# Optimization experiments

Hardware: AMD Instinct MI355X
Metric: run time of the kernel (lower is better)

## Reference

```python
import jax, jax.numpy as jnp
import numpy as np

NUM_HEADS = 8
RMS_EPS = 1e-8


def rmsnorm(x, g):
    return x * jax.lax.rsqrt(jnp.mean(x * x, axis=-1, keepdims=True) + RMS_EPS) * g


def activation_quant(x):
    # per-token int8 absmax quant
    scale = 127.0 / jnp.clip(jnp.max(jnp.abs(x), axis=-1, keepdims=True), 1e-5)
    return jnp.clip(jnp.round(x * scale), -128, 127) / scale


def weight_quant(w):
    # ternary (1.58-bit) mean-absmax quant
    scale = 1.0 / jnp.clip(jnp.mean(jnp.abs(w)), 1e-5)
    return jnp.clip(jnp.round(w * scale), -1, 1) / scale


def bitlinear(x, w, g):
    # BitLinear: RMSNorm -> STE-quantized activation @ STE-quantized ternary weight
    xn = rmsnorm(x, g)
    xq = xn + jax.lax.stop_gradient(activation_quant(xn) - xn)
    wq = w + jax.lax.stop_gradient(weight_quant(w) - w)
    return xq @ wq.T


def _attention_pass(q_in, ctx, Wq, gq, Wkv, gkv, A, Bm, mag, Wp, gp):
    B, Nq, C = q_in.shape
    H = NUM_HEADS
    hd = C // H
    scale = hd ** -0.5
    q_proj = bitlinear(q_in, Wq, gq)                       # [B,Nq,C]
    delta = (q_in @ A.T) @ Bm.T                            # DoRA low-rank delta [B,Nq,C]
    q = q_proj.reshape(B, Nq, H, hd).transpose(0, 2, 1, 3)  # [B,H,Nq,hd]
    d = delta.reshape(B, Nq, H, hd).transpose(0, 2, 1, 3)
    q_final = q + mag * d                                  # mag: [1,H,1,1]
    kv = bitlinear(ctx, Wkv, gkv)                          # [B,Nc,2C]
    k, v = jnp.split(kv, 2, axis=-1)
    Nc = ctx.shape[1]
    k = k.reshape(B, Nc, H, hd).transpose(0, 2, 1, 3)
    v = v.reshape(B, Nc, H, hd).transpose(0, 2, 1, 3)
    scores = jnp.einsum('bhqd,bhkd->bhqk', q_final, k) * scale
    out = jnp.einsum('bhqk,bhkd->bhqd', jax.nn.softmax(scores, axis=-1), v)
    out = out.transpose(0, 2, 1, 3).reshape(B, Nq, C)
    return bitlinear(out, Wp, gp)


def setup_inputs() -> dict:
    key = jax.random.key(0)
    ks = jax.random.split(key, 20)
    B, Nx, Nc, D, R = 4, 4096, 1024, 512, 16
    H = NUM_HEADS

    def rn(k, shape, s=0.02):
        return jax.random.normal(k, shape, dtype=jnp.float32) * s

    return {
        'x': jax.random.normal(ks[0], (B, Nx, D), dtype=jnp.float32),
        'c': jax.random.normal(ks[1], (B, Nc, D), dtype=jnp.float32),
        # x-queries-on-c pass
        'W_qx': rn(ks[2], (D, D)), 'g_qx': jnp.ones((D,), jnp.float32),
        'W_kvc': rn(ks[3], (2 * D, D)), 'g_kvc': jnp.ones((D,), jnp.float32),
        'A_x': rn(ks[4], (R, D)), 'B_x': rn(ks[5], (D, R)),
        'mag_x': jnp.ones((1, H, 1, 1), jnp.float32),
        'W_px': rn(ks[6], (D, D)), 'g_px': jnp.ones((D,), jnp.float32),
        # c-queries-on-x pass
        'W_qc': rn(ks[7], (D, D)), 'g_qc': jnp.ones((D,), jnp.float32),
        'W_kvx': rn(ks[8], (2 * D, D)), 'g_kvx': jnp.ones((D,), jnp.float32),
        'A_c': rn(ks[9], (R, D)), 'B_c': rn(ks[10], (D, R)),
        'mag_c': jnp.ones((1, H, 1, 1), jnp.float32),
        'W_pc': rn(ks[11], (D, D)), 'g_pc': jnp.ones((D,), jnp.float32),
    }


def reference(x, c, W_qx, g_qx, W_kvc, g_kvc, A_x, B_x, mag_x, W_px, g_px,
              W_qc, g_qc, W_kvx, g_kvx, A_c, B_c, mag_c, W_pc, g_pc):
    x_out = x + _attention_pass(x, c, W_qx, g_qx, W_kvc, g_kvc, A_x, B_x, mag_x, W_px, g_px)
    c_out = c + _attention_pass(c, x, W_qc, g_qc, W_kvx, g_kvx, A_c, B_c, mag_c, W_pc, g_pc)
    return (x_out, c_out)
```

## Files before the change

### kernel.cpp

```cpp
#include <hip/hip_runtime.h>
#include <math.h>

#define DD 512
#define NHEAD 8
#define HDIM 64

typedef __bf16 bf16x8 __attribute__((ext_vector_type(8)));
typedef unsigned short u16x8 __attribute__((ext_vector_type(8)));
typedef float f32x4 __attribute__((ext_vector_type(4)));
typedef int i32x4 __attribute__((ext_vector_type(4)));
typedef signed char i8x8 __attribute__((ext_vector_type(8)));

#if __has_builtin(__builtin_amdgcn_exp2f)
#define EXP2F(x) __builtin_amdgcn_exp2f(x)
#else
#define EXP2F(x) exp2f(x)
#endif

#define QSCALE 0.18033688f

static __device__ __forceinline__ unsigned short f2bf(float f) {
    unsigned u = __builtin_bit_cast(unsigned, f);
    u += 0x7fffu + ((u >> 16) & 1u);
    return (unsigned short)(u >> 16);
}
static __device__ __forceinline__ float bf2f(unsigned short u) {
    return __builtin_bit_cast(float, (unsigned)u << 16);
}

static __device__ __forceinline__ float wsum32(const float* __restrict__ part, int mid) {
    int l = threadIdx.x & 63;
    float v = (l < 32) ? part[mid * 32 + l] : 0.f;
#pragma unroll
    for (int o = 16; o > 0; o >>= 1) v += __shfl_xor(v, o);
    return __shfl(v, 0);
}

#define GLOAD16(g, l)                                                          \
    __builtin_amdgcn_global_load_lds(                                          \
        (__attribute__((address_space(1))) void*)(g),                          \
        (__attribute__((address_space(3))) void*)(l), 16, 0, 0)

#define BSTEP(s, hc)                                                           \
    {                                                                          \
        _Pragma("unroll")                                                      \
        for (int i = 0; i < (hc); ++i) {                                       \
            float send = (lane & (s)) ? p[i] : p[i + (hc)];                    \
            float recv = __shfl_xor(send, (s));                                \
            p[i] = ((lane & (s)) ? p[i + (hc)] : p[i]) + recv;                 \
        }                                                                      \
    }

#define ISSUE_TILE(Aq, Wq, m0, n0, k0, slot)                                   \
    {                                                                          \
        _Pragma("unroll")                                                      \
        for (int i = 0; i < 2; ++i)                                            \
            GLOAD16(Aq + (size_t)((m0) + i * 128 + row_st) * 512 + (k0) + chunk * 16, \
                    sA[slot] + ((size_t)i * 512 + t) * 16);                    \
        GLOAD16(Wq + (size_t)((n0) + row_st) * 512 + (k0) + chunk * 16,        \
                sB[slot] + (size_t)t * 16);                                    \
    }

#define GEMM_KLOOP_I8(Aq, Wq, m0, n0)                                          \
    {                                                                          \
        ISSUE_TILE(Aq, Wq, m0, n0, 0, 0)                                       \
        ISSUE_TILE(Aq, Wq, m0, n0, 64, 1)                                      \
        asm volatile("s_waitcnt vmcnt(3)" ::: "memory");                       \
        __builtin_amdgcn_s_barrier();                                          \
        _Pragma("unroll")                                                      \
        for (int step = 0; step < 8; ++step) {                                 \
            if (step + 2 < 8)                                                  \
                ISSUE_TILE(Aq, Wq, m0, n0, (step + 2) * 64, (step + 2) % 3)    \
            const int cs = step % 3;                                           \
            i32x4 af[4], bfr[4];                                               \
            _Pragma("unroll")                                                  \
            for (int mt = 0; mt < 4; ++mt)                                     \
                af[mt] = *reinterpret_cast<const i32x4*>(                      \
                    &sA[cs][(wm * 64 + mt * 16 + lr) * 64 + lg * 16]);         \
            _Pragma("unroll")                                                  \
            for (int nt = 0; nt < 4; ++nt)                                     \
                bfr[nt] = *reinterpret_cast<const i32x4*>(                     \
                    &sB[cs][(wn * 64 + nt * 16 + lr) * 64 + lg * 16]);         \
            __builtin_amdgcn_s_setprio(1);                                     \
            _Pragma("unroll")                                                  \
            for (int mt = 0; mt < 4; ++mt)                                     \
                _Pragma("unroll")                                              \
                for (int nt = 0; nt < 4; ++nt)                                 \
                    acc[mt][nt] = __builtin_amdgcn_mfma_i32_16x16x64_i8(       \
                        af[mt], bfr[nt], acc[mt][nt], 0, 0, 0);                \
            __builtin_amdgcn_s_setprio(0);                                     \
            if (step < 7) {                                                    \
                if (step < 6)                                                  \
                    asm volatile("s_waitcnt vmcnt(3)" ::: "memory");           \
                else                                                           \
                    asm volatile("s_waitcnt vmcnt(0)" ::: "memory");           \
                __builtin_amdgcn_s_barrier();                                  \
            }                                                                  \
        }                                                                      \
    }

__global__ __launch_bounds__(256) void k_prep1(
    const float* __restrict__ W0, const float* __restrict__ W1,
    const float* __restrict__ W2, const float* __restrict__ W3,
    const float* __restrict__ W4, const float* __restrict__ W5,
    float* __restrict__ part,
    const float* __restrict__ x, const float* __restrict__ c,
    const float* __restrict__ g_qx, const float* __restrict__ g_kvx,
    const float* __restrict__ g_qc, const float* __restrict__ g_kvc,
    signed char* __restrict__ a_xq, signed char* __restrict__ a_xkv,
    signed char* __restrict__ a_cq, signed char* __restrict__ a_ckv,
    float* __restrict__ s_xq, float* __restrict__ s_xkv,
    float* __restrict__ s_cq, float* __restrict__ s_ckv,
    const float* __restrict__ A_x, const float* __restrict__ A_c,
    float* __restrict__ tmp_x, float* __restrict__ tmp_c) {
    int t = threadIdx.x;
    if (blockIdx.x < 192) {
        const float* Ws[6] = {W0, W1, W2, W3, W4, W5};
        const int cnt[6] = {262144, 524288, 262144, 262144, 524288, 262144};
        int mid = blockIdx.x >> 5, lb = blockIdx.x & 31;
        const float* W = Ws[mid];
        int n = cnt[mid];
        float s = 0.f;
        for (int i = lb * 256 + t; i < n; i += 32 * 256) s += fabsf(W[i]);
        __shared__ float red[4];
#pragma unroll
        for (int o = 32; o > 0; o >>= 1) s += __shfl_down(s, o);
        if ((t & 63) == 0) red[t >> 6] = s;
        __syncthreads();
        if (t == 0) part[blockIdx.x] = red[0] + red[1] + red[2] + red[3];
        return;
    }
    int w = t >> 6, lane = t & 63;
    int row = (int)(blockIdx.x - 192) * 4 + w;
    bool pc = (row >= 16384);
    int r = pc ? row - 16384 : row;
    const float* xr = (pc ? c : x) + (size_t)r * DD;
    const float* G1 = pc ? g_qc : g_qx;
    const float* G2 = pc ? g_kvc : g_kvx;
    signed char* O1 = pc ? a_cq : a_xq;
    signed char* O2 = pc ? a_ckv : a_xkv;
    float* S1 = pc ? s_cq : s_xq;
    float* S2 = pc ? s_ckv : s_xkv;
    const float* AM = pc ? A_c : A_x;
    float* TMP = pc ? tmp_c : tmp_x;

    float4 a = *(const float4*)(xr + lane * 8);
    float4 b = *(const float4*)(xr + lane * 8 + 4);
    float p[16];
#pragma unroll
    for (int cc = 0; cc < 16; ++cc) {
        const float4* ar = (const float4*)(AM + (size_t)cc * DD + lane * 8);
        float4 aa = ar[0], ab = ar[1];
        p[cc] = a.x*aa.x + a.y*aa.y + a.z*aa.z + a.w*aa.w
              + b.x*ab.x + b.y*ab.y + b.z*ab.z + b.w*ab.w;
    }
    BSTEP(1, 8) BSTEP(2, 4) BSTEP(4, 2) BSTEP(8, 1)
    p[0] += __shfl_xor(p[0], 16);
    p[0] += __shfl_xor(p[0], 32);
    if (lane < 16) {
        int cidx = ((lane & 1) << 3) | ((lane & 2) << 1) | ((lane & 4) >> 1) | ((lane & 8) >> 3);
        TMP[(size_t)r * 16 + cidx] = p[0];
    }
    float ss = a.x*a.x + a.y*a.y + a.z*a.z + a.w*a.w
             + b.x*b.x + b.y*b.y + b.z*b.z + b.w*b.w;
#pragma unroll
    for (int o = 32; o > 0; o >>= 1) ss += __shfl_xor(ss, o);
    float rn = 1.f / sqrtf(ss * (1.f / 512.f) + 1e-8f);
    const float* gs[2] = {G1, G2};
    signed char* os[2] = {O1, O2};
    float* scs[2] = {S1, S2};
#pragma unroll
    for (int pass = 0; pass < 2; ++pass) {
        float4 ga = *(const float4*)(gs[pass] + lane * 8);
        float4 gb = *(const float4*)(gs[pass] + lane * 8 + 4);
        float v[8] = {a.x*rn*ga.x, a.y*rn*ga.y, a.z*rn*ga.z, a.w*rn*ga.w,
                      b.x*rn*gb.x, b.y*rn*gb.y, b.z*rn*gb.z, b.w*rn*gb.w};
        float amax = 0.f;
#pragma unroll
        for (int i = 0; i < 8; ++i) amax = fmaxf(amax, fabsf(v[i]));
#pragma unroll
        for (int o = 32; o > 0; o >>= 1) amax = fmaxf(amax, __shfl_xor(amax, o));
        float mx = fmaxf(amax, 1e-5f);
        float scale = 127.f / mx;
        i8x8 qv;
#pragma unroll
        for (int i = 0; i < 8; ++i) {
            float tq = rintf(v[i] * scale);
            tq = fminf(fmaxf(tq, -128.f), 127.f);
            qv[i] = (signed char)(int)tq;
        }
        *reinterpret_cast<i8x8*>(os[pass] + (size_t)r * DD + lane * 8) = qv;
        if (lane == 0) scs[pass][r] = mx / 127.f;
    }
}

__global__ __launch_bounds__(256) void k_prep2(
    const float* __restrict__ W0, const float* __restrict__ W1,
    const float* __restrict__ W2, const float* __restrict__ W3,
    const float* __restrict__ W4, const float* __restrict__ W5,
    const float* __restrict__ part, signed char* __restrict__ Wq,
    const float* __restrict__ tmp_x, const float* __restrict__ tmp_c,
    const float* __restrict__ B_x, const float* __restrict__ B_c,
    unsigned short* __restrict__ qf1, unsigned short* __restrict__ qf2) {
    if (blockIdx.x < 8192) {
        int e = blockIdx.x * 256 + threadIdx.x;
        const float* Ws[6] = {W0, W1, W2, W3, W4, W5};
        int mid, base;
        if (e < 262144)       { mid = 0; base = 0; }
        else if (e < 786432)  { mid = 1; base = 262144; }
        else if (e < 1048576) { mid = 2; base = 786432; }
        else if (e < 1310720) { mid = 3; base = 1048576; }
        else if (e < 1835008) { mid = 4; base = 1310720; }
        else                  { mid = 5; base = 1835008; }
        float cnt = (mid == 1 || mid == 4) ? 524288.f : 262144.f;
        float mean = fmaxf(wsum32(part, mid) / cnt, 1e-5f);
        float sc = 1.f / mean;
        float t = rintf(Ws[mid][e - base] * sc);
        t = fminf(fmaxf(t, -1.f), 1.f);
        Wq[e] = (signed char)(int)t;
        return;
    }
    int idx = (int)(blockIdx.x - 8192) * 256 + threadIdx.x;
    int m2 = idx >> 9, n2 = idx & 511;
    const float* tr;
    const float* br;
    unsigned short* out;
    if (m2 < 16384) {
        tr = tmp_x + (size_t)m2 * 16; br = B_x + (size_t)n2 * 16; out = qf1 + idx;
    } else {
        tr = tmp_c + (size_t)(m2 - 16384) * 16; br = B_c + (size_t)n2 * 16;
        out = qf2 + (idx - 8388608);
    }
    const float4* t4 = (const float4*)tr;
    const float4* b4 = (const float4*)br;
    float acc = 0.f;
#pragma unroll
    for (int rr = 0; rr < 4; ++rr) {
        float4 ta = t4[rr], ba = b4[rr];
        acc += ta.x*ba.x + ta.y*ba.y + ta.z*ba.z + ta.w*ba.w;
    }
    *out = f2bf(acc);
}

__global__ __launch_bounds__(256) void k_rmsq_combine(
    const unsigned short* __restrict__ Op_a, const float* __restrict__ Lp_a,
    const float* __restrict__ g_a, signed char* __restrict__ out_a,
    float* __restrict__ sc_a,
    const unsigned short* __restrict__ Op_b, const float* __restrict__ Lp_b,
    const float* __restrict__ g_b, signed char* __restrict__ out_b,
    float* __restrict__ sc_b) {
    int w = threadIdx.x >> 6, lane = threadIdx.x & 63;
    int row = (int)blockIdx.x * 4 + w;
    bool pb = (row >= 16384);
    int r = pb ? row - 16384 : row;
    int S = pb ? 4 : 1;
    int lognq = pb ? 10 : 12;
    const unsigned short* Op = pb ? Op_b : Op_a;
    const float* Lp = pb ? Lp_b : Lp_a;
    const float* g  = pb ? g_b : g_a;
    signed char* out = pb ? out_b : out_a;
    float* a_inv = pb ? sc_b : sc_a;

    int Nq = 1 << lognq;
    int b = r >> lognq, q = r & (Nq - 1);
    int h = lane >> 3;
    float l = 0.f;
    float u[8] = {};
    for (int s = 0; s < S; ++s) {
        l += Lp[((size_t)(s * 4 + b) * 8 + h) * Nq + q];
        u16x8 ov = *reinterpret_cast<const u16x8*>(
            Op + ((size_t)(s * 4 + b) * Nq + q) * 512 + lane * 8);
#pragma unroll
        for (int i = 0; i < 8; ++i) u[i] += bf2f(ov[i]);
    }
    float invl = 1.f / l;
#pragma unroll
    for (int i = 0; i < 8; ++i) u[i] *= invl;
    float ss = 0.f;
#pragma unroll
    for (int i = 0; i < 8; ++i) ss += u[i] * u[i];
#pragma unroll
    for (int o = 32; o > 0; o >>= 1) ss += __shfl_xor(ss, o);
    float rn = 1.f / sqrtf(ss * (1.f / 512.f) + 1e-8f);
    float4 ga = *(const float4*)(g + lane * 8);
    float4 gb = *(const float4*)(g + lane * 8 + 4);
    float v[8] = {u[0]*rn*ga.x, u[1]*rn*ga.y, u[2]*rn*ga.z, u[3]*rn*ga.w,
                  u[4]*rn*gb.x, u[5]*rn*gb.y, u[6]*rn*gb.z, u[7]*rn*gb.w};
    float amax = 0.f;
#pragma unroll
    for (int i = 0; i < 8; ++i) amax = fmaxf(amax, fabsf(v[i]));
#pragma unroll
    for (int o = 32; o > 0; o >>= 1) amax = fmaxf(amax, __shfl_xor(amax, o));
    float mx = fmaxf(amax, 1e-5f);
    float scale = 127.f / mx;
    i8x8 qv;
#pragma unroll
    for (int i = 0; i < 8; ++i) {
        float tq = rintf(v[i] * scale);
        tq = fminf(fmaxf(tq, -128.f), 127.f);
        qv[i] = (signed char)(int)tq;
    }
    *reinterpret_cast<i8x8*>(out + (size_t)r * DD + lane * 8) = qv;
    if (lane == 0) a_inv[r] = mx / 127.f;
}

__global__ __launch_bounds__(512) void k_gemm_qkv(
    const signed char* __restrict__ a3_a, const signed char* __restrict__ a3_b,
    const signed char* __restrict__ w3_a, const signed char* __restrict__ w3_b,
    const float* __restrict__ ai3_a, const float* __restrict__ ai3_b,
    const float* __restrict__ mag_a, const float* __restrict__ mag_b,
    const unsigned short* __restrict__ dl_a, const unsigned short* __restrict__ dl_b,
    unsigned short* __restrict__ Qb_a, unsigned short* __restrict__ Qb_b,
    const signed char* __restrict__ a4_a, const signed char* __restrict__ a4_b,
    const signed char* __restrict__ w4_a, const signed char* __restrict__ w4_b,
    const float* __restrict__ ai4_a, const float* __restrict__ ai4_b,
    unsigned short* __restrict__ Kb_a, unsigned short* __restrict__ Kb_b,
    unsigned short* __restrict__ Vt_a, unsigned short* __restrict__ Vt_b,
    const float* __restrict__ part) {
    __shared__ __align__(16) unsigned char sA[3][256 * 64];
    __shared__ __align__(16) unsigned char sB[3][128 * 64];
    int bid = blockIdx.x;
    bool isQ = (bid >= 640);
    const signed char *Aq, *Wq;
    const float* a_inv;
    int m0, n0, logn, mid;
    float cnt;
    bool pb;
    if (!isQ) {
        int g = bid & 7, k = bid >> 3;
        n0 = (k & 7) * 128;
        int my = (k >> 3) * 8 + g;
        pb = my >= 16;
        m0 = (pb ? my - 16 : my) * 256;
        Aq = pb ? a4_b : a4_a;  Wq = pb ? w4_b : w4_a;
        a_inv = pb ? ai4_b : ai4_a;
        logn = pb ? 12 : 10;
        mid = pb ? 4 : 1; cnt = 524288.f;
    } else {
        int b2 = bid - 640;
        int g = b2 & 7, k = b2 >> 3;
        n0 = (k & 3) * 128;
        int my = (k >> 2) * 8 + g;
        pb = my >= 64;
        m0 = (pb ? my - 64 : my) * 256;
        Aq = pb ? a3_b : a3_a;  Wq = pb ? w3_b : w3_a;
        a_inv = pb ? ai3_b : ai3_a;
        logn = pb ? 10 : 12;
        mid = pb ? 3 : 0; cnt = 262144.f;
    }
    float wv = fmaxf(wsum32(part, mid) / cnt, 1e-5f);

    int t = threadIdx.x;
    int w = t >> 6, lane = t & 63;
    int wm = w >> 1, wn = w & 1;
    int lr = lane & 15, lg = lane >> 4;
    int row_st = t >> 2, chunk = t & 3;
    i32x4 acc[4][4] = {};

    GEMM_KLOOP_I8(Aq, Wq, m0, n0)

    if (!isQ) {
        unsigned short* OutB = pb ? Kb_b : Kb_a;
        unsigned short* OutB2 = pb ? Vt_b : Vt_a;
        const bool isV = (n0 >= 512);
        const int Nc = 1 << logn;
#pragma unroll
        for (int mt = 0; mt < 4; ++mt) {
            int mb = m0 + wm * 64 + mt * 16 + lg * 4;
            int b = mb >> logn, key = mb & (Nc - 1);
            float as_[4];
#pragma unroll
            for (int r = 0; r < 4; ++r) as_[r] = a_inv[mb + r] * wv;
#pragma unroll
            for (int nt = 0; nt < 4; ++nt) {
                int n = n0 + wn * 64 + nt * 16 + lr;
                int n2 = isV ? (n - 512) : n;
                int h = n2 >> 6, dd = n2 & 63;
                if (isV) {
                    int i0 = key & 31;
                    int keyp = (key & ~31) | (((i0 >> 2) & 3) * 8 + ((i0 >> 4) & 1) * 4);
                    ushort4 v;
                    v.x = f2bf((float)acc[mt][nt][0] * as_[0]);
                    v.y = f2bf((float)acc[mt][nt][1] * as_[1]);
                    v.z = f2bf((float)acc[mt][nt][2] * as_[2]);
                    v.w = f2bf((float)acc[mt][nt][3] * as_[3]);
                    *reinterpret_cast<ushort4*>(
                        OutB2 + ((size_t)(b * NHEAD + h) * 64 + dd) * Nc + keyp) = v;
                } else {
#pragma unroll
                    for (int r = 0; r < 4; ++r)
                        OutB[((size_t)(b * NHEAD + h) * Nc + key + r) * 64 + dd] =
                            f2bf((float)acc[mt][nt][r] * as_[r]);
                }
            }
        }
    } else {
        const float* Extra = pb ? mag_b : mag_a;
        const unsigned short* Dlt = pb ? dl_b : dl_a;
        unsigned short* OutB = pb ? Qb_b : Qb_a;
#pragma unroll
        for (int mt = 0; mt < 4; ++mt) {
#pragma unroll
            for (int r = 0; r < 4; ++r) {
                int m = m0 + wm * 64 + mt * 16 + lg * 4 + r;
                float as = a_inv[m] * wv;
                int b = m >> logn, q = m & ((1 << logn) - 1);
#pragma unroll
                for (int nt = 0; nt < 4; ++nt) {
                    int n = n0 + wn * 64 + nt * 16 + lr;
                    float dl = bf2f(Dlt[(size_t)m * 512 + n]);
                    float val = (float)acc[mt][nt][r] * as + Extra[n >> 6] * dl;
                    int h = n >> 6, d = n & 63;
                    OutB[((((size_t)(b * NHEAD + h)) << logn) + q) * 64 + d] =
                        f2bf(val * QSCALE);
                }
            }
        }
    }
}

__global__ __launch_bounds__(512) void k_gemm_out(
    const signed char* __restrict__ a_a, const signed char* __restrict__ a_b,
    const signed char* __restrict__ w_a, const signed char* __restrict__ w_b,
    const float* __restrict__ ai_a, const float* __restrict__ ai_b,
    const float* __restrict__ part,
    const float* __restrict__ Ex_a, const float* __restrict__ Ex_b,
    float* __restrict__ OF_a, float* __restrict__ OF_b) {
    __shared__ __align__(16) unsigned char sA[3][256 * 64];
    __shared__ __align__(16) unsigned char sB[3][128 * 64];
    int bid = blockIdx.x;
    int g = bid & 7, k = bid >> 3;
    int n0 = (k & 3) * 128;
    int my = (k >> 2) * 8 + g;
    bool pb = (my >= 64);
    int m0 = (pb ? my - 64 : my) * 256;
    const signed char* Aq = pb ? a_b : a_a;
    const signed char* Wq = pb ? w_b : w_a;
    const float* a_inv = pb ? ai_b : ai_a;
    const float* Extra = pb ? Ex_b : Ex_a;
    float* OutF = pb ? OF_b : OF_a;
    float wv = fmaxf(wsum32(part, pb ? 5 : 2) / 262144.f, 1e-5f);

    int t = threadIdx.x;
    int w = t >> 6, lane = t & 63;
    int wm = w >> 1, wn = w & 1;
    int lr = lane & 15, lg = lane >> 4;
    int row_st = t >> 2, chunk = t & 3;
    i32x4 acc[4][4] = {};

    GEMM_KLOOP_I8(Aq, Wq, m0, n0)

#pragma unroll
    for (int mt = 0; mt < 4; ++mt) {
#pragma unroll
        for (int r = 0; r < 4; ++r) {
            int m = m0 + wm * 64 + mt * 16 + lg * 4 + r;
            float as = a_inv[m] * wv;
#pragma unroll
            for (int nt = 0; nt < 4; ++nt) {
                int n = n0 + wn * 64 + nt * 16 + lr;
                size_t idx = (size_t)m * 512 + n;
                OutF[idx] = (float)acc[mt][nt][r] * as + Extra[idx];
            }
        }
    }
}

__global__ __launch_bounds__(512) void k_attn_mfma(
    const unsigned short* __restrict__ Qb_a, const unsigned short* __restrict__ Kb_a,
    const unsigned short* __restrict__ Vt_a, unsigned short* __restrict__ Op_a,
    float* __restrict__ Lp_a,
    const unsigned short* __restrict__ Qb_b, const unsigned short* __restrict__ Kb_b,
    const unsigned short* __restrict__ Vt_b, unsigned short* __restrict__ Op_b,
    float* __restrict__ Lp_b) {
    __shared__ unsigned short sK[2][64][72];
    __shared__ unsigned short sVt[2][64][72];
    int t = threadIdx.x;
    int w = t >> 6, lane = t & 63;
    int lr = lane & 15, lg = lane >> 4;

    int bid = blockIdx.x;
    bool pb = (bid < 512);
    int lb = pb ? bid : bid - 512;
    const unsigned short* Qb = pb ? Qb_b : Qb_a;
    const unsigned short* Kb = pb ? Kb_b : Kb_a;
    const unsigned short* Vt = pb ? Vt_b : Vt_a;
    unsigned short* Opart = pb ? Op_b : Op_a;
    float* Lpart = pb ? Lp_b : Lp_a;
    int Nq = pb ? 1024 : 4096;
    int Nc = pb ? 4096 : 1024;
    int S = pb ? 4 : 1;
    int LOGS = pb ? 2 : 0;
    int nqs = pb ? 2 : 4;

    int j = lb >> 3;
    int s = j & (S - 1);
    int j2 = j >> LOGS;
    int qblk = j2 & ((1 << nqs) - 1);
    int bh = ((lb & 7) << 2) | (j2 >> nqs);
    int b = bh >> 3, h = bh & 7;
    int q0 = qblk * 256 + w * 32;

    bf16x8 aq[2][2];
#pragma unroll
    for (int qt = 0; qt < 2; ++qt) {
        const unsigned short* qbase = Qb + ((size_t)bh * Nq + q0 + qt * 16 + lr) * 64 + lg * 8;
        aq[qt][0] = *reinterpret_cast<const bf16x8*>(qbase);
        aq[qt][1] = *reinterpret_cast<const bf16x8*>(qbase + 32);
    }

    u16x8 ou;
#pragma unroll
    for (int jj = 0; jj < 8; ++jj) ou[jj] = (lr == 0) ? 0x3F80 : 0;
    bf16x8 onesf = __builtin_bit_cast(bf16x8, ou);

    f32x4 o[2][4] = {};
    f32x4 osum[2] = {};

    const unsigned short* kglob = Kb + (size_t)bh * Nc * 64;
    const unsigned short* vglob = Vt + (size_t)bh * 64 * (size_t)Nc;

    int srow = t >> 3, sseg = t & 7;
    const unsigned short* kptr = kglob + (size_t)srow * 64 + sseg * 8;
    const unsigned short* vptr = vglob + (size_t)srow * Nc + sseg * 8;

    int kts = s * (Nc >> LOGS);
    int nt = (Nc >> LOGS) >> 6;

    bf16x8 rK = *reinterpret_cast<const bf16x8*>(kptr + (size_t)kts * 64);
    bf16x8 rV = *reinterpret_cast<const bf16x8*>(vptr + kts);
    *reinterpret_cast<bf16x8*>(&sK[0][srow][sseg * 8]) = rK;
    *reinterpret_cast<bf16x8*>(&sVt[0][srow][sseg * 8]) = rV;
    rK = *reinterpret_cast<const bf16x8*>(kptr + (size_t)(kts + 64) * 64);
    rV = *reinterpret_cast<const bf16x8*>(vptr + kts + 64);
    __syncthreads();

    int cur = 0;
    for (int ti = 0; ti < nt; ++ti) {
        if (ti + 1 < nt) {
            *reinterpret_cast<bf16x8*>(&sK[cur ^ 1][srow][sseg * 8]) = rK;
            *reinterpret_cast<bf16x8*>(&sVt[cur ^ 1][srow][sseg * 8]) = rV;
            if (ti + 2 < nt) {
                int knext = kts + (ti + 2) * 64;
                rK = *reinterpret_cast<const bf16x8*>(kptr + (size_t)knext * 64);
                rV = *reinterpret_cast<const bf16x8*>(vptr + knext);
            }
        }
#pragma unroll
        for (int half = 0; half < 2; ++half) {
            bf16x8 pa0, pa1;
#pragma unroll
            for (int ki = 0; ki < 2; ++ki) {
                int kt = half * 2 + ki;
                bf16x8 bk0 = *reinterpret_cast<const bf16x8*>(&sK[cur][kt * 16 + lr][lg * 8]);
                bf16x8 bk1 = *reinterpret_cast<const bf16x8*>(&sK[cur][kt * 16 + lr][32 + lg * 8]);
                f32x4 a0 = {}, a1 = {};
                __builtin_amdgcn_s_setprio(1);
                a0 = __builtin_amdgcn_mfma_f32_16x16x32_bf16(bk0, aq[0][0], a0, 0, 0, 0);
                a1 = __builtin_amdgcn_mfma_f32_16x16x32_bf16(bk0, aq[1][0], a1, 0, 0, 0);
                a0 = __builtin_amdgcn_mfma_f32_16x16x32_bf16(bk1, aq[0][1], a0, 0, 0, 0);
                a1 = __builtin_amdgcn_mfma_f32_16x16x32_bf16(bk1, aq[1][1], a1, 0, 0, 0);
                __builtin_amdgcn_s_setprio(0);
                const int hb = ki * 4;
#pragma unroll
                for (int r = 0; r < 4; ++r) {
                    pa0[hb + r] = (__bf16)EXP2F(a0[r]);
                    pa1[hb + r] = (__bf16)EXP2F(a1[r]);
                }
            }
            __builtin_amdgcn_s_setprio(1);
#pragma unroll
            for (int dt = 0; dt < 4; ++dt) {
                bf16x8 vb = *reinterpret_cast<const bf16x8*>(&sVt[cur][dt * 16 + lr][half * 32 + lg * 8]);
                o[0][dt] = __builtin_amdgcn_mfma_f32_16x16x32_bf16(pa0, vb, o[0][dt], 0, 0, 0);
                o[1][dt] = __builtin_amdgcn_mfma_f32_16x16x32_bf16(pa1, vb, o[1][dt], 0, 0, 0);
            }
            osum[0] = __builtin_amdgcn_mfma_f32_16x16x32_bf16(pa0, onesf, osum[0], 0, 0, 0);
            osum[1] = __builtin_amdgcn_mfma_f32_16x16x32_bf16(pa1, onesf, osum[1], 0, 0, 0);
            __builtin_amdgcn_s_setprio(0);
        }
        __syncthreads();
        cur ^= 1;
    }
    unsigned short* obase = Opart + ((size_t)(s * 4 + b) * Nq + q0) * 512 + h * 64;
#pragma unroll
    for (int qt = 0; qt < 2; ++qt)
#pragma unroll
        for (int dt = 0; dt < 4; ++dt)
#pragma unroll
            for (int r = 0; r < 4; ++r)
                obase[(size_t)(qt * 16 + lg * 4 + r) * 512 + dt * 16 + lr] = f2bf(o[qt][dt][r]);
    if (lr == 0) {
        float* lbase = Lpart + ((size_t)(s * 4 + b) * 8 + h) * Nq + q0;
#pragma unroll
        for (int qt = 0; qt < 2; ++qt)
#pragma unroll
            for (int r = 0; r < 4; ++r)
                lbase[qt * 16 + lg * 4 + r] = osum[qt][r];
    }
}

extern "C" void kernel_launch(void* const* d_in, const int* in_sizes, int n_in,
                              void* d_out, int out_size, void* d_ws, size_t ws_size,
                              hipStream_t stream) {
    const float* x     = (const float*)d_in[0];
    const float* c     = (const float*)d_in[1];
    const float* Wq_x  = (const float*)d_in[2];
    const float* g_qx  = (const float*)d_in[3];
    const float* Wkv_c = (const float*)d_in[4];
    const float* g_kvc = (const float*)d_in[5];
    const float* A_x   = (const float*)d_in[6];
    const float* B_x   = (const float*)d_in[7];
    const float* mag_x = (const float*)d_in[8];
    const float* Wp_x  = (const float*)d_in[9];
    const float* g_px  = (const float*)d_in[10];
    const float* Wq_c  = (const float*)d_in[11];
    const float* g_qc  = (const float*)d_in[12];
    const float* Wkv_x = (const float*)d_in[13];
    const float* g_kvx = (const float*)d_in[14];
    const float* A_c   = (const float*)d_in[15];
    const float* B_c   = (const float*)d_in[16];
    const float* mag_c = (const float*)d_in[17];
    const float* Wp_c  = (const float*)d_in[18];
    const float* g_pc  = (const float*)d_in[19];

    float* ws = (float*)d_ws;
    signed char* Wb = (signed char*)ws;
    const size_t Woff[6] = {0, 262144, 786432, 1048576, 1310720, 1835008};
    float* part  = ws + 1048576;
    float* sc_xq  = ws + 1049600;
    float* sc_xkv = sc_xq + 16384;
    float* sc_cq  = sc_xkv + 16384;
    float* sc_ckv = sc_cq + 4096;
    float* sc_o1  = sc_ckv + 4096;
    float* sc_o2  = sc_o1 + 16384;
    float* tmp_x  = ws + 1111040;
    float* tmp_c  = tmp_x + 262144;
    float* actblk = ws + 1438720;
    signed char* act_xq  = (signed char*)actblk;
    signed char* act_xkv = (signed char*)(actblk + 4194304);
    signed char* act_cq  = (signed char*)(actblk + 8388608);
    signed char* act_ckv = (signed char*)(actblk + 9437184);
    unsigned short* Opart1 = (unsigned short*)actblk;
    float* qf1_f  = ws + 11924480;
    unsigned short* Opart2 = (unsigned short*)qf1_f;
    float* qf2_f  = ws + 16118784;
    float* Qb1_f  = ws + 17167360;
    float* Qb2_f  = ws + 21361664;
    float* Kb1_f  = ws + 22410240;
    float* Vt1_f  = ws + 23458816;
    float* Kb2_f  = ws + 24507392;
    float* Vt2_f  = ws + 28701696;
    float* Lpart1 = ws + 32896000;
    float* Lpart2 = ws + 33027072;

    unsigned short* qf1 = (unsigned short*)qf1_f;
    unsigned short* qf2 = (unsigned short*)qf2_f;
    unsigned short* Qb1 = (unsigned short*)Qb1_f;
    unsigned short* Qb2 = (unsigned short*)Qb2_f;
    unsigned short* Kb1 = (unsigned short*)Kb1_f;
    unsigned short* Vt1 = (unsigned short*)Vt1_f;
    unsigned short* Kb2 = (unsigned short*)Kb2_f;
    unsigned short* Vt2 = (unsigned short*)Vt2_f;
    signed char* act_o1 = (signed char*)Qb1;
    signed char* act_o2 = (signed char*)Qb2;

    size_t need = (size_t)33158144 * sizeof(float);
    if (ws_size < need) return;

    float* outx = (float*)d_out;
    float* outc = outx + (size_t)4 * 4096 * 512;

    k_prep1<<<5312, 256, 0, stream>>>(Wq_x, Wkv_c, Wp_x, Wq_c, Wkv_x, Wp_c, part,
                                      x, c, g_qx, g_kvx, g_qc, g_kvc,
                                      act_xq, act_xkv, act_cq, act_ckv,
                                      sc_xq, sc_xkv, sc_cq, sc_ckv,
                                      A_x, A_c, tmp_x, tmp_c);
    k_prep2<<<49152, 256, 0, stream>>>(Wq_x, Wkv_c, Wp_x, Wq_c, Wkv_x, Wp_c, part, Wb,
                                       tmp_x, tmp_c, B_x, B_c, qf1, qf2);
    k_gemm_qkv<<<960, 512, 0, stream>>>(
        act_xq, act_cq, Wb + Woff[0], Wb + Woff[3], sc_xq, sc_cq,
        mag_x, mag_c, qf1, qf2, Qb1, Qb2,
        act_ckv, act_xkv, Wb + Woff[1], Wb + Woff[4], sc_ckv, sc_xkv,
        Kb1, Kb2, Vt1, Vt2, part);
    k_attn_mfma<<<1024, 512, 0, stream>>>(Qb1, Kb1, Vt1, Opart1, Lpart1,
                                          Qb2, Kb2, Vt2, Opart2, Lpart2);
    k_rmsq_combine<<<5120, 256, 0, stream>>>(Opart1, Lpart1, g_px, act_o1, sc_o1,
                                             Opart2, Lpart2, g_pc, act_o2, sc_o2);
    k_gemm_out<<<320, 512, 0, stream>>>(
        act_o1, act_o2, Wb + Woff[2], Wb + Woff[5], sc_o1, sc_o2, part,
        x, c, outx, outc);
}
```

Before: 234.8 us.

## Double per-wave query rows in attention and compute softmax sums with VALU

Each wave now handles 64 query rows (four 16-row subtiles) instead of 32, halving the block count and reusing each K/V tile from shared memory across twice as many queries. The row-sum of exponentials is accumulated in registers with adds and cross-lane shuffles instead of extra MFMAs against a ones vector. Launch bounds request two blocks per CU. The cost is much higher register pressure (16 output accumulators plus 8 query fragments), which may cause spills or lower occupancy, and fewer blocks to balance across CUs.

```diff
diff --git a/kernel.cpp b/kernel.cpp
--- a/kernel.cpp
+++ b/kernel.cpp
@@ -466,7 +466,7 @@
     }
 }
 
-__global__ __launch_bounds__(512) void k_attn_mfma(
+__global__ __launch_bounds__(512, 2) void k_attn_mfma(
     const unsigned short* __restrict__ Qb_a, const unsigned short* __restrict__ Kb_a,
     const unsigned short* __restrict__ Vt_a, unsigned short* __restrict__ Op_a,
     float* __restrict__ Lp_a,
@@ -480,8 +480,8 @@
     int lr = lane & 15, lg = lane >> 4;
 
     int bid = blockIdx.x;
-    bool pb = (bid < 512);
-    int lb = pb ? bid : bid - 512;
+    bool pb = (bid < 256);
+    int lb = pb ? bid : bid - 256;
     const unsigned short* Qb = pb ? Qb_b : Qb_a;
     const unsigned short* Kb = pb ? Kb_b : Kb_a;
     const unsigned short* Vt = pb ? Vt_b : Vt_a;
@@ -491,7 +491,7 @@
     int Nc = pb ? 4096 : 1024;
     int S = pb ? 4 : 1;
     int LOGS = pb ? 2 : 0;
-    int nqs = pb ? 2 : 4;
+    int nqs = pb ? 1 : 3;
 
     int j = lb >> 3;
     int s = j & (S - 1);
@@ -499,23 +499,18 @@
     int qblk = j2 & ((1 << nqs) - 1);
     int bh = ((lb & 7) << 2) | (j2 >> nqs);
     int b = bh >> 3, h = bh & 7;
-    int q0 = qblk * 256 + w * 32;
-
-    bf16x8 aq[2][2];
-#pragma unroll
-    for (int qt = 0; qt < 2; ++qt) {
-        const unsigned short* qbase = Qb + ((size_t)bh * Nq + q0 + qt * 16 + lr) * 64 + lg * 8;
-        aq[qt][0] = *reinterpret_cast<const bf16x8*>(qbase);
-        aq[qt][1] = *reinterpret_cast<const bf16x8*>(qbase + 32);
-    }
-
-    u16x8 ou;
-#pragma unroll
-    for (int jj = 0; jj < 8; ++jj) ou[jj] = (lr == 0) ? 0x3F80 : 0;
-    bf16x8 onesf = __builtin_bit_cast(bf16x8, ou);
-
-    f32x4 o[2][4] = {};
-    f32x4 osum[2] = {};
+    int q0 = qblk * 512 + w * 64;
+
+    bf16x8 aq[4][2];
+#pragma unroll
+    for (int st = 0; st < 4; ++st) {
+        const unsigned short* qbase = Qb + ((size_t)bh * Nq + q0 + st * 16 + lr) * 64 + lg * 8;
+        aq[st][0] = *reinterpret_cast<const bf16x8*>(qbase);
+        aq[st][1] = *reinterpret_cast<const bf16x8*>(qbase + 32);
+    }
+
+    f32x4 o[4][4] = {};
+    float psum[4] = {0.f, 0.f, 0.f, 0.f};
 
     const unsigned short* kglob = Kb + (size_t)bh * Nc * 64;
     const unsigned short* vglob = Vt + (size_t)bh * 64 * (size_t)Nc;
@@ -548,55 +543,64 @@
         }
 #pragma unroll
         for (int half = 0; half < 2; ++half) {
-            bf16x8 pa0, pa1;
+            bf16x8 pa[4];
 #pragma unroll
             for (int ki = 0; ki < 2; ++ki) {
                 int kt = half * 2 + ki;
                 bf16x8 bk0 = *reinterpret_cast<const bf16x8*>(&sK[cur][kt * 16 + lr][lg * 8]);
                 bf16x8 bk1 = *reinterpret_cast<const bf16x8*>(&sK[cur][kt * 16 + lr][32 + lg * 8]);
-                f32x4 a0 = {}, a1 = {};
+                f32x4 a0 = {}, a1 = {}, a2 = {}, a3 = {};
                 __builtin_amdgcn_s_setprio(1);
                 a0 = __builtin_amdgcn_mfma_f32_16x16x32_bf16(bk0, aq[0][0], a0, 0, 0, 0);
                 a1 = __builtin_amdgcn_mfma_f32_16x16x32_bf16(bk0, aq[1][0], a1, 0, 0, 0);
+                a2 = __builtin_amdgcn_mfma_f32_16x16x32_bf16(bk0, aq[2][0], a2, 0, 0, 0);
+                a3 = __builtin_amdgcn_mfma_f32_16x16x32_bf16(bk0, aq[3][0], a3, 0, 0, 0);
                 a0 = __builtin_amdgcn_mfma_f32_16x16x32_bf16(bk1, aq[0][1], a0, 0, 0, 0);
                 a1 = __builtin_amdgcn_mfma_f32_16x16x32_bf16(bk1, aq[1][1], a1, 0, 0, 0);
+                a2 = __builtin_amdgcn_mfma_f32_16x16x32_bf16(bk1, aq[2][1], a2, 0, 0, 0);
+                a3 = __builtin_amdgcn_mfma_f32_16x16x32_bf16(bk1, aq[3][1], a3, 0, 0, 0);
                 __builtin_amdgcn_s_setprio(0);
                 const int hb = ki * 4;
 #pragma unroll
                 for (int r = 0; r < 4; ++r) {
-                    pa0[hb + r] = (__bf16)EXP2F(a0[r]);
-                    pa1[hb + r] = (__bf16)EXP2F(a1[r]);
+                    float e0 = EXP2F(a0[r]); psum[0] += e0; pa[0][hb + r] = (__bf16)e0;
+                    float e1 = EXP2F(a1[r]); psum[1] += e1; pa[1][hb + r] = (__bf16)e1;
+                    float e2 = EXP2F(a2[r]); psum[2] += e2; pa[2][hb + r] = (__bf16)e2;
+                    float e3 = EXP2F(a3[r]); psum[3] += e3; pa[3][hb + r] = (__bf16)e3;
                 }
             }
             __builtin_amdgcn_s_setprio(1);
 #pragma unroll
             for (int dt = 0; dt < 4; ++dt) {
                 bf16x8 vb = *reinterpret_cast<const bf16x8*>(&sVt[cur][dt * 16 + lr][half * 32 + lg * 8]);
-                o[0][dt] = __builtin_amdgcn_mfma_f32_16x16x32_bf16(pa0, vb, o[0][dt], 0, 0, 0);
-                o[1][dt] = __builtin_amdgcn_mfma_f32_16x16x32_bf16(pa1, vb, o[1][dt], 0, 0, 0);
+                o[0][dt] = __builtin_amdgcn_mfma_f32_16x16x32_bf16(pa[0], vb, o[0][dt], 0, 0, 0);
+                o[1][dt] = __builtin_amdgcn_mfma_f32_16x16x32_bf16(pa[1], vb, o[1][dt], 0, 0, 0);
+                o[2][dt] = __builtin_amdgcn_mfma_f32_16x16x32_bf16(pa[2], vb, o[2][dt], 0, 0, 0);
+                o[3][dt] = __builtin_amdgcn_mfma_f32_16x16x32_bf16(pa[3], vb, o[3][dt], 0, 0, 0);
             }
-            osum[0] = __builtin_amdgcn_mfma_f32_16x16x32_bf16(pa0, onesf, osum[0], 0, 0, 0);
-            osum[1] = __builtin_amdgcn_mfma_f32_16x16x32_bf16(pa1, onesf, osum[1], 0, 0, 0);
             __builtin_amdgcn_s_setprio(0);
         }
         __syncthreads();
         cur ^= 1;
     }
+#pragma unroll
+    for (int st = 0; st < 4; ++st) {
+        psum[st] += __shfl_xor(psum[st], 16);
+        psum[st] += __shfl_xor(psum[st], 32);
+    }
     unsigned short* obase = Opart + ((size_t)(s * 4 + b) * Nq + q0) * 512 + h * 64;
 #pragma unroll
-    for (int qt = 0; qt < 2; ++qt)
+    for (int st = 0; st < 4; ++st)
 #pragma unroll
         for (int dt = 0; dt < 4; ++dt)
 #pragma unroll
             for (int r = 0; r < 4; ++r)
-                obase[(size_t)(qt * 16 + lg * 4 + r) * 512 + dt * 16 + lr] = f2bf(o[qt][dt][r]);
-    if (lr == 0) {
+                obase[(size_t)(st * 16 + lg * 4 + r) * 512 + dt * 16 + lr] = f2bf(o[st][dt][r]);
+    if (lane < 16) {
         float* lbase = Lpart + ((size_t)(s * 4 + b) * 8 + h) * Nq + q0;
 #pragma unroll
-        for (int qt = 0; qt < 2; ++qt)
-#pragma unroll
-            for (int r = 0; r < 4; ++r)
-                lbase[qt * 16 + lg * 4 + r] = osum[qt][r];
+        for (int st = 0; st < 4; ++st)
+            lbase[st * 16 + lr] = psum[st];
     }
 }
 
@@ -683,8 +687,8 @@
         mag_x, mag_c, qf1, qf2, Qb1, Qb2,
         act_ckv, act_xkv, Wb + Woff[1], Wb + Woff[4], sc_ckv, sc_xkv,
         Kb1, Kb2, Vt1, Vt2, part);
-    k_attn_mfma<<<1024, 512, 0, stream>>>(Qb1, Kb1, Vt1, Opart1, Lpart1,
-                                          Qb2, Kb2, Vt2, Opart2, Lpart2);
+    k_attn_mfma<<<512, 512, 0, stream>>>(Qb1, Kb1, Vt1, Opart1, Lpart1,
+                                         Qb2, Kb2, Vt2, Opart2, Lpart2);
     k_rmsq_combine<<<5120, 256, 0, stream>>>(Opart1, Lpart1, g_px, act_o1, sc_o1,
                                              Opart2, Lpart2, g_pc, act_o2, sc_o2);
     k_gemm_out<<<320, 512, 0, stream>>>(
```

Result: no change. 236.3 us (+0.6%).
